# Optimization experiments

Hardware: AMD Instinct MI355X
Metric: run time of the kernel (lower is better)

The kernel has to match this reference:

```python
import jax, jax.numpy as jnp
import numpy as np

N = 50000      # nodes
E = 800000     # edges
D_IN = 128
D_H = 128      # dim_h
D_OUT = 1
G = 64         # graphs in batch


def _glorot(key, fan_in, fan_out):
    return jax.random.normal(key, (fan_in, fan_out), jnp.float32) / np.sqrt(fan_in)


def setup_inputs() -> dict:
    key = jax.random.key(0)
    ks = jax.random.split(key, 12)
    x = jax.random.normal(ks[0], (N, D_IN), jnp.float32)
    edge_index = jax.random.randint(ks[1], (2, E), 0, N, dtype=jnp.int32)
    batch = jnp.sort(jax.random.randint(ks[2], (N,), 0, G, dtype=jnp.int32))
    # SAGEConv params: lin_l (bias) on aggregated neighbors, lin_r (no bias) on root
    Wl1 = _glorot(ks[3], D_IN, 2 * D_H); bl1 = jnp.zeros((2 * D_H,), jnp.float32)
    Wr1 = _glorot(ks[4], D_IN, 2 * D_H)
    Wl2 = _glorot(ks[5], 2 * D_H, D_H); bl2 = jnp.zeros((D_H,), jnp.float32)
    Wr2 = _glorot(ks[6], 2 * D_H, D_H)
    Wl3 = _glorot(ks[7], D_H, 16); bl3 = jnp.zeros((16,), jnp.float32)
    Wr3 = _glorot(ks[8], D_H, 16)
    Wc = _glorot(ks[9], 16, D_OUT); bc = jnp.zeros((D_OUT,), jnp.float32)
    return dict(x=x, edge_index=edge_index, batch=batch,
                Wl1=Wl1, bl1=bl1, Wr1=Wr1,
                Wl2=Wl2, bl2=bl2, Wr2=Wr2,
                Wl3=Wl3, bl3=bl3, Wr3=Wr3,
                Wc=Wc, bc=bc)


def _segment_mean(vals, ids, num_segments):
    s = jax.ops.segment_sum(vals, ids, num_segments=num_segments)
    cnt = jax.ops.segment_sum(jnp.ones((vals.shape[0], 1), vals.dtype), ids,
                              num_segments=num_segments)
    return s / jnp.maximum(cnt, 1.0)


def _sage_conv(x, src, dst, Wl, bl, Wr):
    # PyG SAGEConv (mean aggr): lin_l(mean_{j in N(i)} x_j) + lin_r(x_i)
    mean_nbr = _segment_mean(x[src], dst, x.shape[0])  # gather + segment-mean
    return mean_nbr @ Wl + bl + x @ Wr


def reference(x, edge_index, batch,
              Wl1, bl1, Wr1, Wl2, bl2, Wr2, Wl3, bl3, Wr3, Wc, bc):
    src, dst = edge_index[0], edge_index[1]
    h = jax.nn.relu(_sage_conv(x, src, dst, Wl1, bl1, Wr1))   # [N, 256]
    # dropout p=0.5 skipped (training=False)
    h = jax.nn.relu(_sage_conv(h, src, dst, Wl2, bl2, Wr2))   # [N, 128]
    # dropout p=0.2 skipped (training=False)
    h = _sage_conv(h, src, dst, Wl3, bl3, Wr3)                # [N, 16]
    h_pool = _segment_mean(h, batch, G)                       # global_mean_pool [G,16]
    # final dropout is hardcoded training=True in source -> fixed-key dropout
    keep = jax.random.bernoulli(jax.random.key(42), 0.5, h_pool.shape)
    hd = jnp.where(keep, h_pool * 2.0, 0.0)
    out = (hd @ Wc + bc).reshape(-1)                          # [G*dim_out]
    return out, h_pool
```

## Files before the change

### kernel.cpp

```cpp
#include <hip/hip_runtime.h>
#include <stdint.h>


#define GG 64

typedef __attribute__((ext_vector_type(8))) unsigned short ushort8;
typedef __attribute__((ext_vector_type(8))) short bf16s8;
typedef __attribute__((ext_vector_type(4))) float f32x4;

__device__ __forceinline__ unsigned short rne_bf16(float f) {
  unsigned u = __float_as_uint(f);
  return (unsigned short)((u + 0x7FFFu + ((u >> 16) & 1u)) >> 16);
}
__device__ __forceinline__ float bf2f(unsigned short b) {
  return __uint_as_float(((unsigned)b) << 16);
}

__global__ __launch_bounds__(256) void k_cvtprep(const float* __restrict__ x, unsigned short* __restrict__ xb,
                                                 int n8,
                                                 const float* __restrict__ Wl1, const float* __restrict__ Wr1,
                                                 const float* __restrict__ Wl2, const float* __restrict__ Wr2,
                                                 const float* __restrict__ Wl3, const float* __restrict__ Wr3,
                                                 unsigned short* __restrict__ WT1l, unsigned short* __restrict__ WT1r,
                                                 unsigned short* __restrict__ WT2l, unsigned short* __restrict__ WT2r,
                                                 unsigned short* __restrict__ wc3b) {
  int idx = blockIdx.x * 256 + threadIdx.x;
  if (idx < n8) {
    const float4* p = (const float4*)(x + (size_t)idx * 8);
    float4 v0 = p[0], v1 = p[1];
    ushort8 o;
    o[0] = rne_bf16(v0.x); o[1] = rne_bf16(v0.y); o[2] = rne_bf16(v0.z); o[3] = rne_bf16(v0.w);
    o[4] = rne_bf16(v1.x); o[5] = rne_bf16(v1.y); o[6] = rne_bf16(v1.z); o[7] = rne_bf16(v1.w);
    *(ushort8*)(xb + (size_t)idx * 8) = o;
    return;
  }
  int j = idx - n8;
  if (j < 32768) {
    int k = j >> 8, m = j & 255;
    WT1l[m * 128 + k] = rne_bf16(Wl1[j]);
    WT1r[m * 128 + k] = rne_bf16(Wr1[j]);
  } else if (j < 65536) {
    int q = j - 32768;
    int k = q >> 7, m = q & 127;
    WT2l[m * 256 + k] = rne_bf16(Wl2[q]);
    WT2r[m * 256 + k] = rne_bf16(Wr2[q]);
  } else if (j < 69632) {
    int q = j - 65536;
    int m = q >> 7, k = q & 127;
    float v = (m < 16) ? Wl3[k * 16 + m] : Wr3[k * 16 + (m - 16)];
    wc3b[q] = rne_bf16(v);
  }
}

__global__ __launch_bounds__(256) void k_deg(const int* __restrict__ dst, int* __restrict__ deg, int E4) {
  int i = blockIdx.x * 256 + threadIdx.x;
  if (i >= E4) return;
  int4 d4 = *(const int4*)(dst + i * 4);
  atomicAdd(&deg[d4.x], 1);
  atomicAdd(&deg[d4.y], 1);
  atomicAdd(&deg[d4.z], 1);
  atomicAdd(&deg[d4.w], 1);
}

__global__ __launch_bounds__(256) void k_scan_a(const int* __restrict__ deg, int* __restrict__ off,
                                                int* __restrict__ bsum, int N) {
  __shared__ int ws[256];
  const int tid = threadIdx.x;
  const int base = blockIdx.x * 1024 + tid * 4;
  int v0 = (base + 0 < N) ? deg[base + 0] : 0;
  int v1 = (base + 1 < N) ? deg[base + 1] : 0;
  int v2 = (base + 2 < N) ? deg[base + 2] : 0;
  int v3 = (base + 3 < N) ? deg[base + 3] : 0;
  int s = v0 + v1 + v2 + v3;
  ws[tid] = s;
  __syncthreads();
  for (int d = 1; d < 256; d <<= 1) {
    int t = (tid >= d) ? ws[tid - d] : 0;
    __syncthreads();
    ws[tid] += t;
    __syncthreads();
  }
  int excl = ws[tid] - s;
  if (tid == 255) bsum[blockIdx.x] = ws[255];
  if (base + 0 < N) off[base + 0] = excl;
  if (base + 1 < N) off[base + 1] = excl + v0;
  if (base + 2 < N) off[base + 2] = excl + v0 + v1;
  if (base + 3 < N) off[base + 3] = excl + v0 + v1 + v2;
}

__global__ __launch_bounds__(64) void k_scan_b(int* __restrict__ bsum, int nb) {
  int tid = threadIdx.x;
  int v = (tid < nb) ? bsum[tid] : 0;
  for (int d = 1; d < 64; d <<= 1) {
    int t = __shfl_up(v, d, 64);
    if (tid >= d) v += t;
  }
  if (tid < nb) bsum[tid] = v;
}

__global__ __launch_bounds__(256) void k_scan_c(int* __restrict__ off, int* __restrict__ cur,
                                                const int* __restrict__ bsum,
                                                const int* __restrict__ eidx, int N, int nb) {
  int i = blockIdx.x * 256 + threadIdx.x;
  if (i < N) {
    int b = i >> 10;
    int v = off[i] + ((b > 0) ? bsum[b - 1] : 0);
    off[i] = v;
    cur[i] = v;
    const int4* p = (const int4*)(eidx + (size_t)i * 16);
    int4 a0 = p[0], a1 = p[1], a2 = p[2], a3 = p[3];
    int w = a0.x + a1.y + a2.z + a3.w;
    asm volatile("" :: "v"(w));
  }
  if (i == 0) off[N] = bsum[nb - 1];
}

__global__ __launch_bounds__(256) void k_fill(const int* __restrict__ src, const int* __restrict__ dst,
                                              int* __restrict__ cur, int* __restrict__ eidx, int E) {
  int i = blockIdx.x * 256 + threadIdx.x;
  int e0 = i * 4;
  if (e0 + 3 < E) {
    int4 d4 = *(const int4*)(dst + e0);
    int4 s4 = *(const int4*)(src + e0);
    int p0 = atomicAdd(&cur[d4.x], 1);
    int p1 = atomicAdd(&cur[d4.y], 1);
    int p2 = atomicAdd(&cur[d4.z], 1);
    int p3 = atomicAdd(&cur[d4.w], 1);
    eidx[p0] = s4.x;
    eidx[p1] = s4.y;
    eidx[p2] = s4.z;
    eidx[p3] = s4.w;
  } else {
    for (int e = e0; e < E; ++e) {
      int p = atomicAdd(&cur[dst[e]], 1);
      eidx[p] = src[e];
    }
  }
}

template <int OUTBF>
__global__ __launch_bounds__(256) void k_aggr_b(const unsigned short* __restrict__ feat,
                                                const int* __restrict__ off, const int* __restrict__ eidx,
                                                void* __restrict__ out, int N) {
  int idx = blockIdx.x * 256 + threadIdx.x;
  int n = idx >> 4;
  if (n >= N) return;
  int c = (idx & 15) * 8;
  int b = off[n], e = off[n + 1];
  float s0 = 0.f, s1 = 0.f, s2 = 0.f, s3 = 0.f, s4 = 0.f, s5 = 0.f, s6 = 0.f, s7 = 0.f;
  int j = b;
  for (; j + 3 < e; j += 4) {
    int i0 = eidx[j], i1 = eidx[j + 1], i2 = eidx[j + 2], i3 = eidx[j + 3];
    ushort8 v0 = *(const ushort8*)&feat[(size_t)i0 * 128 + c];
    ushort8 v1 = *(const ushort8*)&feat[(size_t)i1 * 128 + c];
    ushort8 v2 = *(const ushort8*)&feat[(size_t)i2 * 128 + c];
    ushort8 v3 = *(const ushort8*)&feat[(size_t)i3 * 128 + c];
    s0 += bf2f(v0[0]) + bf2f(v1[0]) + bf2f(v2[0]) + bf2f(v3[0]);
    s1 += bf2f(v0[1]) + bf2f(v1[1]) + bf2f(v2[1]) + bf2f(v3[1]);
    s2 += bf2f(v0[2]) + bf2f(v1[2]) + bf2f(v2[2]) + bf2f(v3[2]);
    s3 += bf2f(v0[3]) + bf2f(v1[3]) + bf2f(v2[3]) + bf2f(v3[3]);
    s4 += bf2f(v0[4]) + bf2f(v1[4]) + bf2f(v2[4]) + bf2f(v3[4]);
    s5 += bf2f(v0[5]) + bf2f(v1[5]) + bf2f(v2[5]) + bf2f(v3[5]);
    s6 += bf2f(v0[6]) + bf2f(v1[6]) + bf2f(v2[6]) + bf2f(v3[6]);
    s7 += bf2f(v0[7]) + bf2f(v1[7]) + bf2f(v2[7]) + bf2f(v3[7]);
  }
  for (; j < e; ++j) {
    int sidx = eidx[j];
    ushort8 v = *(const ushort8*)&feat[(size_t)sidx * 128 + c];
    s0 += bf2f(v[0]); s1 += bf2f(v[1]); s2 += bf2f(v[2]); s3 += bf2f(v[3]);
    s4 += bf2f(v[4]); s5 += bf2f(v[5]); s6 += bf2f(v[6]); s7 += bf2f(v[7]);
  }
  float sc = 1.f / fmaxf((float)(e - b), 1.f);
  if (OUTBF) {
    ushort8 o;
    o[0] = rne_bf16(s0 * sc); o[1] = rne_bf16(s1 * sc); o[2] = rne_bf16(s2 * sc); o[3] = rne_bf16(s3 * sc);
    o[4] = rne_bf16(s4 * sc); o[5] = rne_bf16(s5 * sc); o[6] = rne_bf16(s6 * sc); o[7] = rne_bf16(s7 * sc);
    *(ushort8*)&((unsigned short*)out)[(size_t)n * 128 + c] = o;
  } else {
    float* po = &((float*)out)[(size_t)n * 128 + c];
    *(float4*)po = make_float4(s0 * sc, s1 * sc, s2 * sc, s3 * sc);
    *(float4*)(po + 4) = make_float4(s4 * sc, s5 * sc, s6 * sc, s7 * sc);
  }
}

template <int DUAL, int HAS_C0, int HAS_BIAS, int RELU, int OUT_BF16>
__global__ __launch_bounds__(256) void k_mgemm(
    const unsigned short* __restrict__ A1, int K1, const unsigned short* __restrict__ B1,
    const unsigned short* __restrict__ A2, const unsigned short* __restrict__ B2, int K2,
    const float* __restrict__ C0, const float* __restrict__ bias,
    void* __restrict__ Cout, int N, int M) {
  __shared__ unsigned short As[64 * 32];
  __shared__ unsigned short Bs[64 * 32];
  const int tid = threadIdx.x;
  const int row0 = blockIdx.y * 64;
  const int col0 = blockIdx.x * 64;
  const int lane = tid & 63;
  const int w = tid >> 6;
  const int wr = w >> 1, wc = w & 1;
  const int rl = lane & 15, g = lane >> 4;
  const int pos = ((g ^ ((rl >> 1) & 3)) << 3);
  const int srow = tid >> 2;
  const int schunk = tid & 3;
  const int spos = ((schunk ^ ((srow >> 1) & 3)) << 3);

  f32x4 acc00 = {0.f, 0.f, 0.f, 0.f}, acc01 = acc00, acc10 = acc00, acc11 = acc00;

  for (int pass = 0; pass < (DUAL ? 2 : 1); ++pass) {
    const unsigned short* __restrict__ A = pass ? A2 : A1;
    const unsigned short* __restrict__ B = pass ? B2 : B1;
    const int K = pass ? K2 : K1;
    for (int k0 = 0; k0 < K; k0 += 32) {
      {
        int r = row0 + srow;
        ushort8 va = (ushort8)(0);
        if (r < N) va = *(const ushort8*)&A[(size_t)r * K + k0 + schunk * 8];
        *(ushort8*)&As[srow * 32 + spos] = va;
        ushort8 vb = *(const ushort8*)&B[(size_t)(col0 + srow) * K + k0 + schunk * 8];
        *(ushort8*)&Bs[srow * 32 + spos] = vb;
      }
      __syncthreads();
      bf16s8 a0 = *(bf16s8*)&As[(wr * 32 + rl) * 32 + pos];
      bf16s8 a1 = *(bf16s8*)&As[(wr * 32 + 16 + rl) * 32 + pos];
      bf16s8 b0 = *(bf16s8*)&Bs[(wc * 32 + rl) * 32 + pos];
      bf16s8 b1 = *(bf16s8*)&Bs[(wc * 32 + 16 + rl) * 32 + pos];
      acc00 = __builtin_amdgcn_mfma_f32_16x16x32_bf16(a0, b0, acc00, 0, 0, 0);
      acc01 = __builtin_amdgcn_mfma_f32_16x16x32_bf16(a0, b1, acc01, 0, 0, 0);
      acc10 = __builtin_amdgcn_mfma_f32_16x16x32_bf16(a1, b0, acc10, 0, 0, 0);
      acc11 = __builtin_amdgcn_mfma_f32_16x16x32_bf16(a1, b1, acc11, 0, 0, 0);
      __syncthreads();
    }
  }

#pragma unroll
  for (int fi = 0; fi < 2; ++fi)
#pragma unroll
    for (int fj = 0; fj < 2; ++fj) {
      const f32x4 a = fi ? (fj ? acc11 : acc10) : (fj ? acc01 : acc00);
#pragma unroll
      for (int reg = 0; reg < 4; ++reg) {
        int r = row0 + wr * 32 + fi * 16 + g * 4 + reg;
        int c = col0 + wc * 32 + fj * 16 + rl;
        if (r >= N) continue;
        float v = a[reg];
        if (HAS_C0) v += C0[(size_t)r * M + c];
        if (HAS_BIAS) v += bias[c];
        if (RELU) v = fmaxf(v, 0.f);
        if (OUT_BF16) ((unsigned short*)Cout)[(size_t)r * M + c] = rne_bf16(v);
        else ((float*)Cout)[(size_t)r * M + c] = v;
      }
    }
}

__global__ __launch_bounds__(256) void k_mgemm3(const unsigned short* __restrict__ A,
                                                const unsigned short* __restrict__ B,
                                                float* __restrict__ C, int N) {
  __shared__ unsigned short As[128 * 32];
  __shared__ unsigned short Bs[32 * 32];
  const int tid = threadIdx.x;
  const int row0 = blockIdx.x * 128;
  const int lane = tid & 63;
  const int w = tid >> 6;
  const int rl = lane & 15, g = lane >> 4;
  const int pos = ((g ^ ((rl >> 1) & 3)) << 3);

  f32x4 acc00 = {0.f, 0.f, 0.f, 0.f}, acc01 = acc00, acc10 = acc00, acc11 = acc00;

  for (int k0 = 0; k0 < 128; k0 += 32) {
#pragma unroll
    for (int it = 0; it < 2; ++it) {
      int cid = tid + it * 256;
      int row = cid >> 2, ch = cid & 3;
      int r = row0 + row;
      ushort8 va = (ushort8)(0);
      if (r < N) va = *(const ushort8*)&A[(size_t)r * 128 + k0 + ch * 8];
      *(ushort8*)&As[row * 32 + ((ch ^ ((row >> 1) & 3)) << 3)] = va;
    }
    if (tid < 128) {
      int row = tid >> 2, ch = tid & 3;
      ushort8 vb = *(const ushort8*)&B[(size_t)row * 128 + k0 + ch * 8];
      *(ushort8*)&Bs[row * 32 + ((ch ^ ((row >> 1) & 3)) << 3)] = vb;
    }
    __syncthreads();
    bf16s8 a0 = *(bf16s8*)&As[(w * 32 + rl) * 32 + pos];
    bf16s8 a1 = *(bf16s8*)&As[(w * 32 + 16 + rl) * 32 + pos];
    bf16s8 b0 = *(bf16s8*)&Bs[rl * 32 + pos];
    bf16s8 b1 = *(bf16s8*)&Bs[(16 + rl) * 32 + pos];
    acc00 = __builtin_amdgcn_mfma_f32_16x16x32_bf16(a0, b0, acc00, 0, 0, 0);
    acc01 = __builtin_amdgcn_mfma_f32_16x16x32_bf16(a0, b1, acc01, 0, 0, 0);
    acc10 = __builtin_amdgcn_mfma_f32_16x16x32_bf16(a1, b0, acc10, 0, 0, 0);
    acc11 = __builtin_amdgcn_mfma_f32_16x16x32_bf16(a1, b1, acc11, 0, 0, 0);
    __syncthreads();
  }

#pragma unroll
  for (int fi = 0; fi < 2; ++fi)
#pragma unroll
    for (int fj = 0; fj < 2; ++fj) {
      const f32x4 a = fi ? (fj ? acc11 : acc10) : (fj ? acc01 : acc00);
#pragma unroll
      for (int reg = 0; reg < 4; ++reg) {
        int r = row0 + w * 32 + fi * 16 + g * 4 + reg;
        int c = fj * 16 + rl;
        if (r < N) C[(size_t)r * 32 + c] = a[reg];
      }
    }
}

__global__ __launch_bounds__(256) void k_l3post(const float* __restrict__ g3, const int* __restrict__ off,
                                                const int* __restrict__ eidx, const float* __restrict__ bl3,
                                                float* __restrict__ h3, int N) {
  int idx = blockIdx.x * 256 + threadIdx.x;
  int n = idx >> 2;
  if (n >= N) return;
  int c = (idx & 3) << 2;
  int b = off[n], e = off[n + 1];
  float ax = 0.f, ay = 0.f, az = 0.f, aw = 0.f;
  int j = b;
  for (; j + 3 < e; j += 4) {
    int i0 = eidx[j], i1 = eidx[j + 1], i2 = eidx[j + 2], i3 = eidx[j + 3];
    const float4 v0 = *(const float4*)&g3[(size_t)i0 * 32 + c];
    const float4 v1 = *(const float4*)&g3[(size_t)i1 * 32 + c];
    const float4 v2 = *(const float4*)&g3[(size_t)i2 * 32 + c];
    const float4 v3 = *(const float4*)&g3[(size_t)i3 * 32 + c];
    ax += v0.x + v1.x + v2.x + v3.x;
    ay += v0.y + v1.y + v2.y + v3.y;
    az += v0.z + v1.z + v2.z + v3.z;
    aw += v0.w + v1.w + v2.w + v3.w;
  }
  for (; j < e; ++j) {
    int s = eidx[j];
    const float4 v = *(const float4*)&g3[(size_t)s * 32 + c];
    ax += v.x; ay += v.y; az += v.z; aw += v.w;
  }
  float sc = 1.f / fmaxf((float)(e - b), 1.f);
  const float4 r2 = *(const float4*)&g3[(size_t)n * 32 + 16 + c];
  const float4 bb = *(const float4*)&bl3[c];
  *(float4*)&h3[(size_t)n * 16 + c] =
      make_float4(ax * sc + r2.x + bb.x, ay * sc + r2.y + bb.y,
                  az * sc + r2.z + bb.z, aw * sc + r2.w + bb.w);
}

__device__ __forceinline__ int lbound(const int* __restrict__ a, int n, int v) {
  int lo = 0, hi = n;
  while (lo < hi) {
    int mid = (lo + hi) >> 1;
    if (a[mid] < v) lo = mid + 1; else hi = mid;
  }
  return lo;
}

__global__ __launch_bounds__(256) void k_pool(const float* __restrict__ h3, const int* __restrict__ batch,
                                              int N, float* __restrict__ hpool, float* __restrict__ outp) {
  __shared__ float sm[4][16];
  int g = blockIdx.x, tid = threadIdx.x;
  int start = lbound(batch, N, g);
  int end = lbound(batch, N, g + 1);
  float acc[16];
#pragma unroll
  for (int j = 0; j < 16; ++j) acc[j] = 0.f;
  for (int i = start + tid; i < end; i += 256) {
    const float4* p = (const float4*)&h3[(size_t)i * 16];
    float4 v0 = p[0], v1 = p[1], v2 = p[2], v3 = p[3];
    acc[0] += v0.x; acc[1] += v0.y; acc[2] += v0.z; acc[3] += v0.w;
    acc[4] += v1.x; acc[5] += v1.y; acc[6] += v1.z; acc[7] += v1.w;
    acc[8] += v2.x; acc[9] += v2.y; acc[10] += v2.z; acc[11] += v2.w;
    acc[12] += v3.x; acc[13] += v3.y; acc[14] += v3.z; acc[15] += v3.w;
  }
#pragma unroll
  for (int j = 0; j < 16; ++j) {
    float v = acc[j];
    v += __shfl_down(v, 32);
    v += __shfl_down(v, 16);
    v += __shfl_down(v, 8);
    v += __shfl_down(v, 4);
    v += __shfl_down(v, 2);
    v += __shfl_down(v, 1);
    if ((tid & 63) == 0) sm[tid >> 6][j] = v;
  }
  __syncthreads();
  if (tid < 16) {
    float v = sm[0][tid] + sm[1][tid] + sm[2][tid] + sm[3][tid];
    v /= fmaxf((float)(end - start), 1.f);
    hpool[g * 16 + tid] = v;
    outp[g * 16 + tid] = v;
  }
}

__device__ __forceinline__ uint2 tf2x32(unsigned k0, unsigned k1, unsigned x0, unsigned x1) {
  const unsigned ks[3] = {k0, k1, k0 ^ k1 ^ 0x1BD11BDAu};
  const int rotA[4] = {13, 15, 26, 6}, rotB[4] = {17, 29, 16, 24};
  x0 += ks[0];
  x1 += ks[1];
#pragma unroll
  for (int i = 0; i < 5; ++i) {
    const int* R = (i & 1) ? rotB : rotA;
#pragma unroll
    for (int j = 0; j < 4; ++j) {
      x0 += x1;
      x1 = (x1 << R[j]) | (x1 >> (32 - R[j]));
      x1 ^= x0;
    }
    x0 += ks[(i + 1) % 3];
    x1 += ks[(i + 2) % 3] + (unsigned)(i + 1);
  }
  return make_uint2(x0, x1);
}

__global__ __launch_bounds__(1024) void k_final(const float* __restrict__ hpool,
                                                float* __restrict__ outp,
                                                const float* __restrict__ Wc,
                                                const float* __restrict__ bc) {
  int t = threadIdx.x;
  float m = hpool[t];
  uint2 r = tf2x32(0u, 42u, 0u, (unsigned)t);
  unsigned bits = r.x ^ r.y;
  float hd = (bits >> 31) ? 0.f : 2.f * m;
  float contrib = hd * Wc[t & 15];
  contrib += __shfl_down(contrib, 8, 16);
  contrib += __shfl_down(contrib, 4, 16);
  contrib += __shfl_down(contrib, 2, 16);
  contrib += __shfl_down(contrib, 1, 16);
  if ((t & 15) == 0) outp[t >> 4] = contrib + bc[0];
}

extern "C" void kernel_launch(void* const* d_in, const int* in_sizes, int n_in,
                              void* d_out, int out_size, void* d_ws, size_t ws_size,
                              hipStream_t stream) {
  const float* x   = (const float*)d_in[0];
  const int*   ei  = (const int*)d_in[1];
  const int*   bat = (const int*)d_in[2];
  const float* Wl1 = (const float*)d_in[3];
  const float* bl1 = (const float*)d_in[4];
  const float* Wr1 = (const float*)d_in[5];
  const float* Wl2 = (const float*)d_in[6];
  const float* bl2 = (const float*)d_in[7];
  const float* Wr2 = (const float*)d_in[8];
  const float* Wl3 = (const float*)d_in[9];
  const float* bl3 = (const float*)d_in[10];
  const float* Wr3 = (const float*)d_in[11];
  const float* Wc  = (const float*)d_in[12];
  const float* bc  = (const float*)d_in[13];

  const int E = in_sizes[1] / 2;
  const int N = in_sizes[2];
  const int* src = ei;
  const int* dst = ei + E;

  int*   off   = (int*)d_ws;
  int*   deg   = off + 50016;
  int*   bsum  = (int*)d_ws + 100016;
  float* hpool = (float*)d_ws + 100096;
  unsigned short* wc3b = (unsigned short*)((float*)d_ws + 101120);
  unsigned short* WT1l = (unsigned short*)((float*)d_ws + 105216);
  unsigned short* WT1r = (unsigned short*)((float*)d_ws + 121600);
  unsigned short* WT2l = (unsigned short*)((float*)d_ws + 137984);
  unsigned short* WT2r = (unsigned short*)((float*)d_ws + 154368);
  int*   eidx  = (int*)d_ws + 170752;
  unsigned short* xb   = (unsigned short*)((float*)d_ws + 970752);
  unsigned short* aggb = (unsigned short*)((float*)d_ws + 4170752);
  unsigned short* h1b  = (unsigned short*)((float*)d_ws + 7370752);
  unsigned short* t2b  = xb;
  unsigned short* h2b  = (unsigned short*)((float*)d_ws + 970752);
  float* agg2 = (float*)d_ws + 13770752;
  int*   cur  = (int*)agg2;
  float* g3   = (float*)d_ws + 7370752;
  float* h3   = (float*)d_ws + 8970752;
  float* outp = (float*)d_out;

  const int gy = (N + 63) / 64;
  const int gy3 = (N + 127) / 128;
  const int nb = (N + 1023) / 1024;
  const int n8 = N * 128 / 8;

  k_cvtprep<<<(n8 + 69632 + 255) / 256, 256, 0, stream>>>(x, xb, n8, Wl1, Wr1, Wl2, Wr2, Wl3, Wr3,
                                                          WT1l, WT1r, WT2l, WT2r, wc3b);

  hipMemsetAsync(deg, 0, (size_t)N * 4, stream);
  k_deg<<<(E / 4 + 255) / 256, 256, 0, stream>>>(dst, deg, E / 4);
  k_scan_a<<<nb, 256, 0, stream>>>(deg, off, bsum, N);
  k_scan_b<<<1, 64, 0, stream>>>(bsum, nb);
  k_scan_c<<<(N + 255) / 256, 256, 0, stream>>>(off, cur, bsum, eidx, N, nb);
  k_fill<<<((E + 3) / 4 + 255) / 256, 256, 0, stream>>>(src, dst, cur, eidx, E);

  k_aggr_b<1><<<(N * 16 + 255) / 256, 256, 0, stream>>>(xb, off, eidx, aggb, N);
  k_mgemm<1, 0, 1, 1, 1><<<dim3(4, gy), 256, 0, stream>>>(aggb, 128, WT1l, xb, WT1r, 128,
                                                          nullptr, bl1, h1b, N, 256);

  k_mgemm<0, 0, 0, 0, 1><<<dim3(2, gy), 256, 0, stream>>>(h1b, 256, WT2l, nullptr, nullptr, 0,
                                                          nullptr, nullptr, t2b, N, 128);
  k_aggr_b<0><<<(N * 16 + 255) / 256, 256, 0, stream>>>(t2b, off, eidx, agg2, N);
  k_mgemm<0, 1, 1, 1, 1><<<dim3(2, gy), 256, 0, stream>>>(h1b, 256, WT2r, nullptr, nullptr, 0,
                                                          agg2, bl2, h2b, N, 128);

  k_mgemm3<<<gy3, 256, 0, stream>>>(h2b, wc3b, g3, N);
  k_l3post<<<(N * 4 + 255) / 256, 256, 0, stream>>>(g3, off, eidx, bl3, h3, N);

  k_pool<<<GG, 256, 0, stream>>>(h3, bat, N, hpool, outp + 64);
  k_final<<<1, 1024, 0, stream>>>(hpool, outp, Wc, bc);
}
```

Baseline: 248.5 us.

## Partition CSR fill by XCD so each die's L2 owns a destination range

The CSR fill kernel is restructured so blocks are grouped by blockIdx modulo 8, one group per XCD, and each group handles only edges whose destination falls in its slice of the node range. Each block first touches its slice of the eidx array to warm that XCD's L2, replacing the prefetch that used to sit in the scan kernel. The aim is to keep the atomics on cur and the scattered eidx writes local to one die's L2 instead of bouncing across XCDs. In exchange, every group reads the full src/dst edge lists, so edge-list reads grow eightfold, and the scheme relies on blocks being assigned to XCDs round-robin.

```diff
diff --git a/kernel.cpp b/kernel.cpp
--- a/kernel.cpp
+++ b/kernel.cpp
@@ -3,6 +3,7 @@
 
 
 #define GG 64
+#define NXCD 8
 
 typedef __attribute__((ext_vector_type(8))) unsigned short ushort8;
 typedef __attribute__((ext_vector_type(8))) short bf16s8;
@@ -99,42 +100,47 @@
 }
 
 __global__ __launch_bounds__(256) void k_scan_c(int* __restrict__ off, int* __restrict__ cur,
-                                                const int* __restrict__ bsum,
-                                                const int* __restrict__ eidx, int N, int nb) {
+                                                const int* __restrict__ bsum, int N, int nb) {
   int i = blockIdx.x * 256 + threadIdx.x;
   if (i < N) {
     int b = i >> 10;
     int v = off[i] + ((b > 0) ? bsum[b - 1] : 0);
     off[i] = v;
     cur[i] = v;
-    const int4* p = (const int4*)(eidx + (size_t)i * 16);
-    int4 a0 = p[0], a1 = p[1], a2 = p[2], a3 = p[3];
-    int w = a0.x + a1.y + a2.z + a3.w;
-    asm volatile("" :: "v"(w));
   }
   if (i == 0) off[N] = bsum[nb - 1];
 }
 
 __global__ __launch_bounds__(256) void k_fill(const int* __restrict__ src, const int* __restrict__ dst,
-                                              int* __restrict__ cur, int* __restrict__ eidx, int E) {
-  int i = blockIdx.x * 256 + threadIdx.x;
-  int e0 = i * 4;
-  if (e0 + 3 < E) {
+                                              const int* __restrict__ off, int* __restrict__ cur,
+                                              int* __restrict__ eidx, int E, int N, int binsz, int ngrp) {
+  const int xcd = blockIdx.x & (NXCD - 1);
+  const int grp = blockIdx.x >> 3;
+  const int t = grp * 256 + threadIdx.x;
+  const int nthr = ngrp * 256;
+  const int lo = xcd * binsz;
+  const int hi = min(lo + binsz, N);
+
+  int s0 = off[lo] & ~15;
+  int s1 = off[hi];
+  for (int i = s0 + t * 16; i < s1; i += nthr * 16) {
+    int v = eidx[i];
+    asm volatile("" :: "v"(v));
+  }
+
+  int e0 = t * 4;
+  const int stride = nthr * 4;
+  for (; e0 + 3 < E; e0 += stride) {
     int4 d4 = *(const int4*)(dst + e0);
     int4 s4 = *(const int4*)(src + e0);
-    int p0 = atomicAdd(&cur[d4.x], 1);
-    int p1 = atomicAdd(&cur[d4.y], 1);
-    int p2 = atomicAdd(&cur[d4.z], 1);
-    int p3 = atomicAdd(&cur[d4.w], 1);
-    eidx[p0] = s4.x;
-    eidx[p1] = s4.y;
-    eidx[p2] = s4.z;
-    eidx[p3] = s4.w;
-  } else {
-    for (int e = e0; e < E; ++e) {
-      int p = atomicAdd(&cur[dst[e]], 1);
-      eidx[p] = src[e];
-    }
+    if (d4.x >= lo && d4.x < hi) { int p = atomicAdd(&cur[d4.x], 1); eidx[p] = s4.x; }
+    if (d4.y >= lo && d4.y < hi) { int p = atomicAdd(&cur[d4.y], 1); eidx[p] = s4.y; }
+    if (d4.z >= lo && d4.z < hi) { int p = atomicAdd(&cur[d4.z], 1); eidx[p] = s4.z; }
+    if (d4.w >= lo && d4.w < hi) { int p = atomicAdd(&cur[d4.w], 1); eidx[p] = s4.w; }
+  }
+  for (; e0 < E; ++e0) {
+    int d = dst[e0];
+    if (d >= lo && d < hi) { int p = atomicAdd(&cur[d], 1); eidx[p] = src[e0]; }
   }
 }
 
@@ -471,6 +477,8 @@
   const int gy3 = (N + 127) / 128;
   const int nb = (N + 1023) / 1024;
   const int n8 = N * 128 / 8;
+  const int binsz = (N + NXCD - 1) / NXCD;
+  const int ngrp = 96;
 
   k_cvtprep<<<(n8 + 69632 + 255) / 256, 256, 0, stream>>>(x, xb, n8, Wl1, Wr1, Wl2, Wr2, Wl3, Wr3,
                                                           WT1l, WT1r, WT2l, WT2r, wc3b);
@@ -479,8 +487,8 @@
   k_deg<<<(E / 4 + 255) / 256, 256, 0, stream>>>(dst, deg, E / 4);
   k_scan_a<<<nb, 256, 0, stream>>>(deg, off, bsum, N);
   k_scan_b<<<1, 64, 0, stream>>>(bsum, nb);
-  k_scan_c<<<(N + 255) / 256, 256, 0, stream>>>(off, cur, bsum, eidx, N, nb);
-  k_fill<<<((E + 3) / 4 + 255) / 256, 256, 0, stream>>>(src, dst, cur, eidx, E);
+  k_scan_c<<<(N + 255) / 256, 256, 0, stream>>>(off, cur, bsum, N, nb);
+  k_fill<<<ngrp * NXCD, 256, 0, stream>>>(src, dst, off, cur, eidx, E, N, binsz, ngrp);
 
   k_aggr_b<1><<<(N * 16 + 255) / 256, 256, 0, stream>>>(xb, off, eidx, aggb, N);
   k_mgemm<1, 0, 1, 1, 1><<<dim3(4, gy), 256, 0, stream>>>(aggb, 128, WT1l, xb, WT1r, 128,
```

Result: no change. 245.4 us (-1.2%).
